# Kernel optimization log

Measured on AMD Instinct MI355X. Metric: run time of the kernel, lower is better.

## Reference

```python
import jax, jax.numpy as jnp
import numpy as np

N_NODES = 100000
N_EDGES = 3200000
D_FEAT = 128


def setup_inputs() -> dict:
    key = jax.random.key(0)
    k1, k2, k3, k4 = jax.random.split(key, 4)
    rows = jax.random.randint(k1, (N_EDGES,), 0, N_NODES, dtype=jnp.int32)
    cols = jax.random.randint(k2, (N_EDGES,), 0, N_NODES, dtype=jnp.int32)
    vals = jax.random.uniform(k3, (N_EDGES,), dtype=jnp.float32)
    embeds = jax.random.normal(k4, (N_NODES, D_FEAT), dtype=jnp.float32)
    return {"rows": rows, "cols": cols, "vals": vals, "embeds": embeds}


def reference(rows, cols, vals, embeds):
    # out = adj @ embeds, adj in COO form: out[r] += vals[e] * embeds[cols[e]]
    gathered = vals[:, None] * embeds[cols]          # [E, D]
    out = jax.ops.segment_sum(gathered, rows, num_segments=N_NODES)  # [N, D]
    return out
```

## Files before the change

### kernel.cpp

```cpp
#include <hip/hip_runtime.h>

#define D_FEAT  128
#define RSHIFT  6
#define RPB     64
#define NB_MAX  2048
#define NBLK    512
#define BT      256
#define CAP     2432

__global__ void zero_out_kernel(float* __restrict__ out, int n4) {
    int i = blockIdx.x * blockDim.x + threadIdx.x;
    if (i < n4) ((float4*)out)[i] = make_float4(0.f, 0.f, 0.f, 0.f);
}

__global__ void coo_scatter_atomic_kernel(const int* __restrict__ rows,
                                          const int* __restrict__ cols,
                                          const float* __restrict__ vals,
                                          const float* __restrict__ embeds,
                                          float* __restrict__ out,
                                          int n_edges) {
    int tid  = blockIdx.x * blockDim.x + threadIdx.x;
    int edge = tid >> 5;
    int lane = tid & 31;
    if (edge >= n_edges) return;
    int   r = rows[edge];
    int   c = cols[edge];
    float v = vals[edge];
    const float4* src = (const float4*)(embeds + (size_t)c * D_FEAT);
    float4 e = src[lane];
    float* dst = out + (size_t)r * D_FEAT + lane * 4;
    atomicAdd(dst + 0, v * e.x);
    atomicAdd(dst + 1, v * e.y);
    atomicAdd(dst + 2, v * e.z);
    atomicAdd(dst + 3, v * e.w);
}

__device__ inline unsigned short f2bf(float f) {
    unsigned int u = __float_as_uint(f);
    u += 0x7fffu + ((u >> 16) & 1u);
    return (unsigned short)(u >> 16);
}

__global__ __launch_bounds__(256) void conv_bf16_kernel(const float4* __restrict__ in,
                                                        ushort4* __restrict__ out, int n4) {
    int i = blockIdx.x * blockDim.x + threadIdx.x;
    if (i >= n4) return;
    float4 f = in[i];
    ushort4 o;
    o.x = f2bf(f.x); o.y = f2bf(f.y); o.z = f2bf(f.z); o.w = f2bf(f.w);
    out[i] = o;
}


__global__ __launch_bounds__(BT) void p1_count(const int* __restrict__ rows,
                                               int* __restrict__ Cmat,
                                               int n_edges, int nb, int tile) {
    __shared__ int cnt[NB_MAX];
    int blk = blockIdx.x, t = threadIdx.x;
    for (int b = t; b < nb; b += BT) cnt[b] = 0;
    __syncthreads();
    int e0 = blk * tile;
    int e1 = min(e0 + tile, n_edges);
    for (int i = e0 + t; i < e1; i += BT)
        atomicAdd(&cnt[rows[i] >> RSHIFT], 1);
    __syncthreads();
    int* dst = Cmat + (size_t)blk * nb;
    for (int b = t; b < nb; b += BT) dst[b] = cnt[b];
}

__global__ __launch_bounds__(NBLK) void s3_fused(const int* __restrict__ Cmat,
                                                 int* __restrict__ BmatT,
                                                 int* __restrict__ total, int nb) {
    __shared__ int s[NBLK];
    int b = blockIdx.x, t = threadIdx.x;
    int v = Cmat[(size_t)t * nb + b];
    s[t] = v;
    __syncthreads();
    for (int off = 1; off < NBLK; off <<= 1) {
        int u = (t >= off) ? s[t - off] : 0;
        __syncthreads();
        s[t] += u;
        __syncthreads();
    }
    BmatT[(size_t)b * NBLK + t] = s[t] - v;
    if (t == NBLK - 1) total[b] = s[t];
}

__global__ __launch_bounds__(1024) void s2_base(const int* __restrict__ total,
                                                int* __restrict__ base, int nb) {
    __shared__ int s[2048];
    int t = threadIdx.x;
    int v0 = (t < nb) ? total[t] : 0;
    int v1 = (t + 1024 < nb) ? total[t + 1024] : 0;
    s[t] = v0;
    s[t + 1024] = v1;
    __syncthreads();
    for (int off = 1; off < 2048; off <<= 1) {
        int u0 = (t >= off) ? s[t - off] : 0;
        int u1 = (t + 1024 >= off) ? s[t + 1024 - off] : 0;
        __syncthreads();
        s[t] += u0;
        s[t + 1024] += u1;
        __syncthreads();
    }
    if (t < nb)        base[t]        = s[t]        - v0;
    if (t + 1024 < nb) base[t + 1024] = s[t + 1024] - v1;
}

__global__ __launch_bounds__(BT) void p2_scatter(const int* __restrict__ rows,
                                                 const int* __restrict__ cols,
                                                 const float* __restrict__ vals,
                                                 const int* __restrict__ base,
                                                 const int* __restrict__ BmatT,
                                                 int2* __restrict__ pairs,
                                                 int n_edges, int nb, int tile) {
    __shared__ int curs[NB_MAX];
    int blk = blockIdx.x, t = threadIdx.x;
    for (int b = t; b < nb; b += BT)
        curs[b] = base[b] + BmatT[(size_t)b * NBLK + blk];
    __syncthreads();
    int e0 = blk * tile;
    int e1 = min(e0 + tile, n_edges);
    for (int i = e0 + t; i < e1; i += BT) {
        int   r = rows[i];
        int   c = cols[i];
        float v = vals[i];
        int   b = r >> RSHIFT;
        int pos = atomicAdd(&curs[b], 1);
        pairs[pos] = make_int2(c | ((r & (RPB - 1)) << 17), __float_as_int(v));
    }
}

template <bool BF16>
__global__ __launch_bounds__(256) void reduce_bucket_kernel(const int* __restrict__ total,
                                                            const int* __restrict__ base,
                                                            const int2* __restrict__ pairs,
                                                            const float* __restrict__ embF,
                                                            const uint2* __restrict__ embB,
                                                            float* __restrict__ out,
                                                            int n_rows) {
    __shared__ int2 stage[CAP];
    __shared__ int  hist[RPB];
    __shared__ int  rptr[RPB + 1];
    __shared__ int  cur[RPB];
    __shared__ int  scan_s[256];

    int b = blockIdx.x, t = threadIdx.x;
    int n     = total[b];
    int pbase = base[b];
    if (n > CAP) n = CAP;

    if (t < RPB) hist[t] = 0;
    __syncthreads();
    for (int i = t; i < n; i += 256)
        atomicAdd(&hist[(pairs[pbase + i].x >> 17) & (RPB - 1)], 1);
    __syncthreads();
    int hv = (t < RPB) ? hist[t] : 0;
    scan_s[t] = hv;
    __syncthreads();
    for (int off = 1; off < RPB; off <<= 1) {
        int u = (t >= off) ? scan_s[t - off] : 0;
        __syncthreads();
        scan_s[t] += u;
        __syncthreads();
    }
    if (t < RPB) {
        rptr[t + 1] = scan_s[t];
        cur[t]      = scan_s[t] - hv;
    }
    if (t == 0) rptr[0] = 0;
    __syncthreads();

    for (int i = t; i < n; i += 256) {
        int2 p  = pairs[pbase + i];
        int  lr = (p.x >> 17) & (RPB - 1);
        int pos = atomicAdd(&cur[lr], 1);
        stage[pos] = make_int2(p.x & 0x1FFFF, p.y);
    }
    __syncthreads();

    int g    = t >> 5;
    int lane = t & 31;
    int row0 = b << RSHIFT;
    for (int r = g; r < RPB; r += 8) {
        int row = row0 + r;
        if (row >= n_rows) break;
        int s0 = rptr[r], s1 = rptr[r + 1];
        float4 acc = make_float4(0.f, 0.f, 0.f, 0.f);
        int e = s0;
        for (; e + 3 < s1; e += 4) {
            int2 p0 = stage[e];
            int2 p1 = stage[e + 1];
            int2 p2 = stage[e + 2];
            int2 p3 = stage[e + 3];
            float v0 = __int_as_float(p0.y), v1 = __int_as_float(p1.y);
            float v2 = __int_as_float(p2.y), v3 = __int_as_float(p3.y);
            if (BF16) {
                uint2 q0 = embB[(size_t)p0.x * 32 + lane];
                uint2 q1 = embB[(size_t)p1.x * 32 + lane];
                uint2 q2 = embB[(size_t)p2.x * 32 + lane];
                uint2 q3 = embB[(size_t)p3.x * 32 + lane];
                acc.x += v0 * __uint_as_float(q0.x << 16);
                acc.y += v0 * __uint_as_float(q0.x & 0xffff0000u);
                acc.z += v0 * __uint_as_float(q0.y << 16);
                acc.w += v0 * __uint_as_float(q0.y & 0xffff0000u);
                acc.x += v1 * __uint_as_float(q1.x << 16);
                acc.y += v1 * __uint_as_float(q1.x & 0xffff0000u);
                acc.z += v1 * __uint_as_float(q1.y << 16);
                acc.w += v1 * __uint_as_float(q1.y & 0xffff0000u);
                acc.x += v2 * __uint_as_float(q2.x << 16);
                acc.y += v2 * __uint_as_float(q2.x & 0xffff0000u);
                acc.z += v2 * __uint_as_float(q2.y << 16);
                acc.w += v2 * __uint_as_float(q2.y & 0xffff0000u);
                acc.x += v3 * __uint_as_float(q3.x << 16);
                acc.y += v3 * __uint_as_float(q3.x & 0xffff0000u);
                acc.z += v3 * __uint_as_float(q3.y << 16);
                acc.w += v3 * __uint_as_float(q3.y & 0xffff0000u);
            } else {
                const float4* e4 = (const float4*)embF;
                float4 t0 = e4[(size_t)p0.x * 32 + lane];
                float4 t1 = e4[(size_t)p1.x * 32 + lane];
                float4 t2 = e4[(size_t)p2.x * 32 + lane];
                float4 t3 = e4[(size_t)p3.x * 32 + lane];
                acc.x += v0 * t0.x; acc.y += v0 * t0.y; acc.z += v0 * t0.z; acc.w += v0 * t0.w;
                acc.x += v1 * t1.x; acc.y += v1 * t1.y; acc.z += v1 * t1.z; acc.w += v1 * t1.w;
                acc.x += v2 * t2.x; acc.y += v2 * t2.y; acc.z += v2 * t2.z; acc.w += v2 * t2.w;
                acc.x += v3 * t3.x; acc.y += v3 * t3.y; acc.z += v3 * t3.z; acc.w += v3 * t3.w;
            }
        }
        for (; e < s1; ++e) {
            int2 p = stage[e];
            float v = __int_as_float(p.y);
            if (BF16) {
                uint2 q = embB[(size_t)p.x * 32 + lane];
                acc.x += v * __uint_as_float(q.x << 16);
                acc.y += v * __uint_as_float(q.x & 0xffff0000u);
                acc.z += v * __uint_as_float(q.y << 16);
                acc.w += v * __uint_as_float(q.y & 0xffff0000u);
            } else {
                float4 tt = ((const float4*)embF)[(size_t)p.x * 32 + lane];
                acc.x += v * tt.x; acc.y += v * tt.y; acc.z += v * tt.z; acc.w += v * tt.w;
            }
        }
        ((float4*)(out + (size_t)row * D_FEAT))[lane] = acc;
    }
}

extern "C" void kernel_launch(void* const* d_in, const int* in_sizes, int n_in,
                              void* d_out, int out_size, void* d_ws, size_t ws_size,
                              hipStream_t stream) {
    const int*   rows   = (const int*)d_in[0];
    const int*   cols   = (const int*)d_in[1];
    const float* vals   = (const float*)d_in[2];
    const float* embeds = (const float*)d_in[3];
    float*       out    = (float*)d_out;

    const int n_edges = in_sizes[0];
    const int n_rows  = out_size / D_FEAT;
    const int n_nodes = in_sizes[3] / D_FEAT;

    const int nb = (n_rows + RPB - 1) >> RSHIFT;

    size_t cmat_b  = (((size_t)NBLK * nb * sizeof(int)) + 255) & ~(size_t)255;
    size_t bmatT_b = (((size_t)nb * NBLK * sizeof(int)) + 255) & ~(size_t)255;
    size_t tot_b   = (((size_t)nb * sizeof(int)) + 255) & ~(size_t)255;
    size_t base_b  = tot_b;
    size_t pair_b  = (((size_t)n_edges * sizeof(int2)) + 255) & ~(size_t)255;
    size_t embB_b  = (size_t)n_nodes * D_FEAT * sizeof(unsigned short);
    size_t need0   = cmat_b + bmatT_b + tot_b + base_b + pair_b;
    size_t need1   = need0 + embB_b;

    bool ok = (ws_size >= need0) && (nb <= NB_MAX) &&
              (n_nodes <= (1 << 17)) && (n_rows <= (1 << 17));
    if (!ok) {
        int out_n4 = out_size / 4;
        zero_out_kernel<<<(out_n4 + 255) / 256, 256, 0, stream>>>(out, out_n4);
        long long totalT = (long long)n_edges * 32;
        int grid = (int)((totalT + 255) / 256);
        coo_scatter_atomic_kernel<<<grid, 256, 0, stream>>>(rows, cols, vals, embeds, out, n_edges);
        return;
    }
    bool use_bf16 = (ws_size >= need1);

    char* ws = (char*)d_ws;
    int*   Cmat  = (int*)ws;    ws += cmat_b;
    int*   BmatT = (int*)ws;    ws += bmatT_b;
    int*   total = (int*)ws;    ws += tot_b;
    int*   base  = (int*)ws;    ws += base_b;
    int2*  pairs = (int2*)ws;   ws += pair_b;
    uint2* embB  = (uint2*)ws;

    int tile = (n_edges + NBLK - 1) / NBLK;

    if (use_bf16) {
        int n4 = (n_nodes * D_FEAT) / 4;
        conv_bf16_kernel<<<(n4 + 255) / 256, 256, 0, stream>>>((const float4*)embeds,
                                                               (ushort4*)embB, n4);
    }
    p1_count  <<<NBLK, BT,   0, stream>>>(rows, Cmat, n_edges, nb, tile);
    s3_fused  <<<nb,   NBLK, 0, stream>>>(Cmat, BmatT, total, nb);
    s2_base   <<<1,    1024, 0, stream>>>(total, base, nb);
    p2_scatter<<<NBLK, BT,   0, stream>>>(rows, cols, vals, base, BmatT, pairs,
                                          n_edges, nb, tile);
    if (use_bf16)
        reduce_bucket_kernel<true><<<nb, 256, 0, stream>>>(total, base, pairs,
                                                           embeds, embB, out, n_rows);
    else
        reduce_bucket_kernel<false><<<nb, 256, 0, stream>>>(total, base, pairs,
                                                            embeds, embB, out, n_rows);
}
```

Before: 342.9 us.

## Sort bucket edges by column chunk so all blocks sweep embeddings in lockstep

The per-bucket counting sort now keys on both the column chunk (bits 13-16 of the column) and the local row, giving 1024 bins instead of 64. Each warp keeps eight row accumulators in registers and walks the chunks in order, so gathers across concurrently running blocks fall in a narrow slice of the embedding table and hit L2/MALL more often. In exchange it uses more registers (eight float4 accumulators), runs a 256-wide scan instead of 64, and cuts the inner unroll from four to two, which may lower memory-level parallelism and occupancy.

Result: slower. 424.8 us (+23.9%).

```diff
diff --git a/kernel.cpp b/kernel.cpp
--- a/kernel.cpp
+++ b/kernel.cpp
@@ -7,6 +7,10 @@
 #define NBLK    512
 #define BT      256
 #define CAP     2432
+
+#define CHSHIFT 13
+#define NCH     16
+#define BINS    (NCH * RPB)
 
 __global__ void zero_out_kernel(float* __restrict__ out, int n4) {
     int i = blockIdx.x * blockDim.x + threadIdx.x;
@@ -140,9 +144,9 @@
                                                             float* __restrict__ out,
                                                             int n_rows) {
     __shared__ int2 stage[CAP];
-    __shared__ int  hist[RPB];
-    __shared__ int  rptr[RPB + 1];
-    __shared__ int  cur[RPB];
+    __shared__ int  hist[BINS];
+    __shared__ int  rptr[BINS + 1];
+    __shared__ int  cur[BINS];
     __shared__ int  scan_s[256];
 
     int b = blockIdx.x, t = threadIdx.x;
@@ -150,31 +154,40 @@
     int pbase = base[b];
     if (n > CAP) n = CAP;
 
-    if (t < RPB) hist[t] = 0;
-    __syncthreads();
-    for (int i = t; i < n; i += 256)
-        atomicAdd(&hist[(pairs[pbase + i].x >> 17) & (RPB - 1)], 1);
-    __syncthreads();
-    int hv = (t < RPB) ? hist[t] : 0;
-    scan_s[t] = hv;
-    __syncthreads();
-    for (int off = 1; off < RPB; off <<= 1) {
+    for (int i = t; i < BINS; i += 256) hist[i] = 0;
+    __syncthreads();
+    for (int i = t; i < n; i += 256) {
+        int x = pairs[pbase + i].x;
+        int key = (((x >> CHSHIFT) & (NCH - 1)) << RSHIFT) | ((x >> 17) & (RPB - 1));
+        atomicAdd(&hist[key], 1);
+    }
+    __syncthreads();
+    int h0 = hist[4 * t], h1 = hist[4 * t + 1], h2 = hist[4 * t + 2], h3 = hist[4 * t + 3];
+    int local = h0 + h1 + h2 + h3;
+    scan_s[t] = local;
+    __syncthreads();
+    for (int off = 1; off < 256; off <<= 1) {
         int u = (t >= off) ? scan_s[t - off] : 0;
         __syncthreads();
         scan_s[t] += u;
         __syncthreads();
     }
-    if (t < RPB) {
-        rptr[t + 1] = scan_s[t];
-        cur[t]      = scan_s[t] - hv;
-    }
-    if (t == 0) rptr[0] = 0;
+    int base_t = scan_s[t] - local;
+    rptr[4 * t]     = base_t;
+    rptr[4 * t + 1] = base_t + h0;
+    rptr[4 * t + 2] = base_t + h0 + h1;
+    rptr[4 * t + 3] = base_t + h0 + h1 + h2;
+    cur[4 * t]      = base_t;
+    cur[4 * t + 1]  = base_t + h0;
+    cur[4 * t + 2]  = base_t + h0 + h1;
+    cur[4 * t + 3]  = base_t + h0 + h1 + h2;
+    if (t == 255) rptr[BINS] = base_t + local;
     __syncthreads();
 
     for (int i = t; i < n; i += 256) {
         int2 p  = pairs[pbase + i];
-        int  lr = (p.x >> 17) & (RPB - 1);
-        int pos = atomicAdd(&cur[lr], 1);
+        int key = (((p.x >> CHSHIFT) & (NCH - 1)) << RSHIFT) | ((p.x >> 17) & (RPB - 1));
+        int pos = atomicAdd(&cur[key], 1);
         stage[pos] = make_int2(p.x & 0x1FFFF, p.y);
     }
     __syncthreads();
@@ -182,67 +195,65 @@
     int g    = t >> 5;
     int lane = t & 31;
     int row0 = b << RSHIFT;
-    for (int r = g; r < RPB; r += 8) {
-        int row = row0 + r;
-        if (row >= n_rows) break;
-        int s0 = rptr[r], s1 = rptr[r + 1];
-        float4 acc = make_float4(0.f, 0.f, 0.f, 0.f);
-        int e = s0;
-        for (; e + 3 < s1; e += 4) {
-            int2 p0 = stage[e];
-            int2 p1 = stage[e + 1];
-            int2 p2 = stage[e + 2];
-            int2 p3 = stage[e + 3];
-            float v0 = __int_as_float(p0.y), v1 = __int_as_float(p1.y);
-            float v2 = __int_as_float(p2.y), v3 = __int_as_float(p3.y);
-            if (BF16) {
-                uint2 q0 = embB[(size_t)p0.x * 32 + lane];
-                uint2 q1 = embB[(size_t)p1.x * 32 + lane];
-                uint2 q2 = embB[(size_t)p2.x * 32 + lane];
-                uint2 q3 = embB[(size_t)p3.x * 32 + lane];
-                acc.x += v0 * __uint_as_float(q0.x << 16);
-                acc.y += v0 * __uint_as_float(q0.x & 0xffff0000u);
-                acc.z += v0 * __uint_as_float(q0.y << 16);
-                acc.w += v0 * __uint_as_float(q0.y & 0xffff0000u);
-                acc.x += v1 * __uint_as_float(q1.x << 16);
-                acc.y += v1 * __uint_as_float(q1.x & 0xffff0000u);
-                acc.z += v1 * __uint_as_float(q1.y << 16);
-                acc.w += v1 * __uint_as_float(q1.y & 0xffff0000u);
-                acc.x += v2 * __uint_as_float(q2.x << 16);
-                acc.y += v2 * __uint_as_float(q2.x & 0xffff0000u);
-                acc.z += v2 * __uint_as_float(q2.y << 16);
-                acc.w += v2 * __uint_as_float(q2.y & 0xffff0000u);
-                acc.x += v3 * __uint_as_float(q3.x << 16);
-                acc.y += v3 * __uint_as_float(q3.x & 0xffff0000u);
-                acc.z += v3 * __uint_as_float(q3.y << 16);
-                acc.w += v3 * __uint_as_float(q3.y & 0xffff0000u);
-            } else {
-                const float4* e4 = (const float4*)embF;
-                float4 t0 = e4[(size_t)p0.x * 32 + lane];
-                float4 t1 = e4[(size_t)p1.x * 32 + lane];
-                float4 t2 = e4[(size_t)p2.x * 32 + lane];
-                float4 t3 = e4[(size_t)p3.x * 32 + lane];
-                acc.x += v0 * t0.x; acc.y += v0 * t0.y; acc.z += v0 * t0.z; acc.w += v0 * t0.w;
-                acc.x += v1 * t1.x; acc.y += v1 * t1.y; acc.z += v1 * t1.z; acc.w += v1 * t1.w;
-                acc.x += v2 * t2.x; acc.y += v2 * t2.y; acc.z += v2 * t2.z; acc.w += v2 * t2.w;
-                acc.x += v3 * t3.x; acc.y += v3 * t3.y; acc.z += v3 * t3.z; acc.w += v3 * t3.w;
+    float4 acc[8];
+#pragma unroll
+    for (int j = 0; j < 8; ++j) acc[j] = make_float4(0.f, 0.f, 0.f, 0.f);
+
+    for (int ch = 0; ch < NCH; ++ch) {
+#pragma unroll
+        for (int j = 0; j < 8; ++j) {
+            int seg = (ch << RSHIFT) | (g + (j << 3));
+            int s0 = rptr[seg], s1 = rptr[seg + 1];
+            int e = s0;
+            for (; e + 1 < s1; e += 2) {
+                int2 p0 = stage[e];
+                int2 p1 = stage[e + 1];
+                float v0 = __int_as_float(p0.y);
+                float v1 = __int_as_float(p1.y);
+                if (BF16) {
+                    uint2 q0 = embB[(size_t)p0.x * 32 + lane];
+                    uint2 q1 = embB[(size_t)p1.x * 32 + lane];
+                    acc[j].x += v0 * __uint_as_float(q0.x << 16);
+                    acc[j].y += v0 * __uint_as_float(q0.x & 0xffff0000u);
+                    acc[j].z += v0 * __uint_as_float(q0.y << 16);
+                    acc[j].w += v0 * __uint_as_float(q0.y & 0xffff0000u);
+                    acc[j].x += v1 * __uint_as_float(q1.x << 16);
+                    acc[j].y += v1 * __uint_as_float(q1.x & 0xffff0000u);
+                    acc[j].z += v1 * __uint_as_float(q1.y << 16);
+                    acc[j].w += v1 * __uint_as_float(q1.y & 0xffff0000u);
+                } else {
+                    const float4* e4 = (const float4*)embF;
+                    float4 t0 = e4[(size_t)p0.x * 32 + lane];
+                    float4 t1 = e4[(size_t)p1.x * 32 + lane];
+                    acc[j].x += v0 * t0.x; acc[j].y += v0 * t0.y;
+                    acc[j].z += v0 * t0.z; acc[j].w += v0 * t0.w;
+                    acc[j].x += v1 * t1.x; acc[j].y += v1 * t1.y;
+                    acc[j].z += v1 * t1.z; acc[j].w += v1 * t1.w;
+                }
+            }
+            if (e < s1) {
+                int2 p = stage[e];
+                float v = __int_as_float(p.y);
+                if (BF16) {
+                    uint2 q = embB[(size_t)p.x * 32 + lane];
+                    acc[j].x += v * __uint_as_float(q.x << 16);
+                    acc[j].y += v * __uint_as_float(q.x & 0xffff0000u);
+                    acc[j].z += v * __uint_as_float(q.y << 16);
+                    acc[j].w += v * __uint_as_float(q.y & 0xffff0000u);
+                } else {
+                    float4 tt = ((const float4*)embF)[(size_t)p.x * 32 + lane];
+                    acc[j].x += v * tt.x; acc[j].y += v * tt.y;
+                    acc[j].z += v * tt.z; acc[j].w += v * tt.w;
+                }
             }
         }
-        for (; e < s1; ++e) {
-            int2 p = stage[e];
-            float v = __int_as_float(p.y);
-            if (BF16) {
-                uint2 q = embB[(size_t)p.x * 32 + lane];
-                acc.x += v * __uint_as_float(q.x << 16);
-                acc.y += v * __uint_as_float(q.x & 0xffff0000u);
-                acc.z += v * __uint_as_float(q.y << 16);
-                acc.w += v * __uint_as_float(q.y & 0xffff0000u);
-            } else {
-                float4 tt = ((const float4*)embF)[(size_t)p.x * 32 + lane];
-                acc.x += v * tt.x; acc.y += v * tt.y; acc.z += v * tt.z; acc.w += v * tt.w;
-            }
-        }
-        ((float4*)(out + (size_t)row * D_FEAT))[lane] = acc;
+    }
+
+#pragma unroll
+    for (int j = 0; j < 8; ++j) {
+        int row = row0 + g + (j << 3);
+        if (row < n_rows)
+            ((float4*)(out + (size_t)row * D_FEAT))[lane] = acc[j];
     }
 }
 
```
